# Kernel optimization log

Measured on AMD Instinct MI355X. Metric: run time of the kernel, lower is better.

## Reference

```python
import jax, jax.numpy as jnp
import numpy as np

# Grid derived from defaults: pc_range=(0,-40,-3,70.4,40,1), voxel=(0.2,0.2,4)
GX, GY = 352, 400          # round((70.4-0)/0.2), round((40-(-40))/0.2)
B, P = 4, 65536            # samples, points per sample
NSEG = B * GX * GY + 1     # dense pillar-id space + 1 sentinel for masked points
OUT_CH = 64
BN_EPS = 1e-3


def setup_inputs() -> dict:
    key = jax.random.key(0)
    k1, k2, k3 = jax.random.split(key, 3)
    xyz_min = jnp.array([0.0, -40.0, -3.0], jnp.float32)
    xyz_max = jnp.array([70.4, 40.0, 1.0], jnp.float32)
    xyz = jax.random.uniform(k1, (B, P, 3), jnp.float32, minval=xyz_min, maxval=xyz_max)
    rest = jax.random.normal(k2, (B, P, 4), jnp.float32)  # rcs, v_r, v_r_comp, time
    points = jnp.concatenate([xyz, rest], axis=-1)        # [B, P, 7]
    W = jax.random.normal(k3, (OUT_CH, 13), jnp.float32) * (1.0 / np.sqrt(13.0))
    gamma = jnp.ones((OUT_CH,), jnp.float32)
    beta = jnp.zeros((OUT_CH,), jnp.float32)
    return {"points": points, "W": W, "gamma": gamma, "beta": beta}


def reference(points, W, gamma, beta):
    Bn, Pn, _ = points.shape
    pts = points.reshape(Bn * Pn, 7)                      # [N, 7] (= torch points[:, 1:])
    dtype = pts.dtype
    voxel = jnp.array([0.2, 0.2, 4.0], dtype)
    pc_min = jnp.array([0.0, -40.0, -3.0], dtype)
    batch_idx = jnp.repeat(jnp.arange(Bn, dtype=jnp.int32), Pn)

    coords_f = (pts[:, :3] - pc_min) / voxel              # float voxel coords
    mask = ((coords_f[:, 0] >= 0) & (coords_f[:, 0] < GX)
            & (coords_f[:, 1] >= 0) & (coords_f[:, 1] < GY))
    coords = coords_f.astype(jnp.int32)                   # [N, 3] (cx, cy, cz)
    sentinel = Bn * GX * GY                               # trash segment for masked points
    lin = jnp.where(mask,
                    batch_idx * (GX * GY) + coords[:, 0] * GY + coords[:, 1],
                    sentinel)
    # torch.unique(..., return_inverse=True, dim=0) on (batch, cx, cy) rows ==
    # unique of the bijective linear id (same sorted order).
    unq, unq_inv = jnp.unique(lin, return_inverse=True, size=NSEG, fill_value=sentinel)

    cnt = jax.ops.segment_sum(jnp.ones((lin.shape[0], 1), dtype), unq_inv, num_segments=NSEG)
    mean_xyz = jax.ops.segment_sum(pts[:, :3], unq_inv, num_segments=NSEG) / jnp.maximum(cnt, 1.0)
    f_cluster = pts[:, :3] - mean_xyz[unq_inv]
    f_center = pts[:, :3] - (coords.astype(dtype) * voxel + voxel * 0.5 + pc_min)
    feats = jnp.concatenate([pts, f_cluster, f_center], axis=-1)   # [N, 13]

    # PFN layer (last_layer=True): Linear -> BN1d (training stats) -> ReLU
    x = feats @ W.T                                       # [N, 64]
    mu = x.mean(axis=0)
    var = x.var(axis=0)                                   # biased, as BN training
    x = jax.nn.relu((x - mu) * jax.lax.rsqrt(var + BN_EPS) * gamma + beta)

    fmax = jax.ops.segment_max(x, unq_inv, num_segments=NSEG)     # scatter_max
    x_max = fmax[unq_inv]                                 # gather back (PFN output)
    feat_max = jax.ops.segment_max(x_max, unq_inv, num_segments=NSEG)

    valid = (unq < sentinel)[:, None]                     # real pillars only
    feat_max = jnp.where(valid, feat_max, 0.0)            # padded/empty -> 0

    b = unq // (GX * GY)
    rem = unq % (GX * GY)
    cx = rem // GY
    cy = rem % GY
    coords_out = jnp.stack([b, cy, cx], axis=1).astype(jnp.int32)  # (batch, y, x)
    grid_size = jnp.array([GY, GX], jnp.int32)
    return feat_max, coords_out, grid_size
```

## Files before the change

### kernel.cpp

```cpp
#include <hip/hip_runtime.h>
#include <stdint.h>
#include <utility>

#define NPTS   262144
#define GXGY   140800
#define GYv    400
#define NSEG   563201
#define SENT   563200
#define NB_SCAN 275
#define PIL_BLOCKS 2048

constexpr size_t alignup(size_t x) { return (x + 255) & ~(size_t)255; }
constexpr size_t O_CNT  = 0;
constexpr size_t O_SUMS = alignup(O_CNT + (size_t)NSEG * 4);
constexpr size_t O_MOM  = alignup(O_SUMS + (size_t)NSEG * 12);
constexpr size_t ZERO_BYTES = alignup(O_MOM + 104 * 4);
constexpr size_t O_PPTR = ZERO_BYTES;
constexpr size_t O_LIST = alignup(O_PPTR + (size_t)NSEG * 4);
constexpr size_t O_LINA = alignup(O_LIST + (size_t)NPTS * 4);
constexpr size_t O_FEAT = alignup(O_LINA + (size_t)NPTS * 4);
constexpr size_t O_BSO  = alignup(O_FEAT + (size_t)NPTS * 64);
constexpr size_t O_BSC  = alignup(O_BSO + NB_SCAN * 4);
constexpr size_t O_BOO  = alignup(O_BSC + NB_SCAN * 4);
constexpr size_t O_BOC  = alignup(O_BOO + NB_SCAN * 4);
constexpr size_t O_KP   = alignup(O_BOC + NB_SCAN * 4);
constexpr size_t O_WF   = alignup(O_KP + 256);
constexpr size_t O_SH   = alignup(O_WF + 832 * 4);

__device__ __forceinline__ int point_lin(float x, float y, int b, bool& mask) {
  float cxf = x / 0.2f;
  float cyf = (y + 40.0f) / 0.2f;
  int cx = (int)cxf, cy = (int)cyf;
  mask = (cxf >= 0.0f) && (cxf < 352.0f) && (cyf >= 0.0f) && (cyf < 400.0f);
  return mask ? (b * GXGY + cx * GYv + cy) : SENT;
}

__global__ __launch_bounds__(256) void k_count(const float* __restrict__ pts,
                                               unsigned int* __restrict__ cnt,
                                               float* __restrict__ sums,
                                               unsigned int* __restrict__ lina) {
  int i = blockIdx.x * 256 + threadIdx.x;
  if (i >= NPTS) return;
  const float* p = pts + (size_t)i * 7;
  float x = p[0], y = p[1], z = p[2];
  bool m;
  int lin = point_lin(x, y, i >> 16, m);
  lina[i] = (unsigned)lin;
  atomicAdd(&cnt[lin], 1u);
  atomicAdd(&sums[lin * 3 + 0], x);
  atomicAdd(&sums[lin * 3 + 1], y);
  atomicAdd(&sums[lin * 3 + 2], z);
}

__global__ __launch_bounds__(256) void k_scan1(const unsigned int* __restrict__ cnt,
                                               unsigned int* __restrict__ bso,
                                               unsigned int* __restrict__ bsc) {
  int t = threadIdx.x;
  int base = blockIdx.x * 2048 + t * 8;
  const uint4* c4 = (const uint4*)(cnt + base);
  uint4 a = c4[0], b = c4[1];
  unsigned so = (a.x > 0) + (a.y > 0) + (a.z > 0) + (a.w > 0) +
                (b.x > 0) + (b.y > 0) + (b.z > 0) + (b.w > 0);
  unsigned sc = a.x + a.y + a.z + a.w + b.x + b.y + b.z + b.w;
  for (int m = 1; m < 64; m <<= 1) { so += __shfl_xor(so, m); sc += __shfl_xor(sc, m); }
  __shared__ unsigned wo[4], wc[4];
  if ((t & 63) == 0) { wo[t >> 6] = so; wc[t >> 6] = sc; }
  __syncthreads();
  if (t == 0) {
    bso[blockIdx.x] = wo[0] + wo[1] + wo[2] + wo[3];
    bsc[blockIdx.x] = wc[0] + wc[1] + wc[2] + wc[3];
  }
}

__global__ __launch_bounds__(512) void k_scan2(const unsigned int* __restrict__ bso,
                                               const unsigned int* __restrict__ bsc,
                                               unsigned int* __restrict__ boo,
                                               unsigned int* __restrict__ boc,
                                               unsigned int* __restrict__ kp) {
  int t = threadIdx.x;
  unsigned vo = (t < NB_SCAN) ? bso[t] : 0u;
  unsigned vc = (t < NB_SCAN) ? bsc[t] : 0u;
  __shared__ unsigned so[512], sc[512];
  so[t] = vo; sc[t] = vc;
  __syncthreads();
  for (int off = 1; off < 512; off <<= 1) {
    unsigned ao = (t >= off) ? so[t - off] : 0u;
    unsigned ac = (t >= off) ? sc[t - off] : 0u;
    __syncthreads();
    so[t] += ao; sc[t] += ac;
    __syncthreads();
  }
  if (t < NB_SCAN) { boo[t] = so[t] - vo; boc[t] = sc[t] - vc; }
  if (t == 511) *kp = so[511];
}

__global__ __launch_bounds__(256) void k_scan3(const unsigned int* __restrict__ cnt,
                                               const unsigned int* __restrict__ boo,
                                               const unsigned int* __restrict__ boc,
                                               unsigned int* __restrict__ list,
                                               unsigned int* __restrict__ pptr) {
  int t = threadIdx.x;
  int base = blockIdx.x * 2048 + t * 8;
  const uint4* q = (const uint4*)(cnt + base);
  uint4 a = q[0], b = q[1];
  unsigned c[8] = {a.x, a.y, a.z, a.w, b.x, b.y, b.z, b.w};
  unsigned po[8], pc[8];
  unsigned so = 0, sc = 0;
#pragma unroll
  for (int k = 0; k < 8; k++) {
    po[k] = so; pc[k] = sc;
    so += (c[k] > 0); sc += c[k];
  }
  __shared__ unsigned sdo[256], sdc[256];
  sdo[t] = so; sdc[t] = sc;
  __syncthreads();
  for (int off = 1; off < 256; off <<= 1) {
    unsigned ao = (t >= off) ? sdo[t - off] : 0u;
    unsigned ac = (t >= off) ? sdc[t - off] : 0u;
    __syncthreads();
    sdo[t] += ao; sdc[t] += ac;
    __syncthreads();
  }
  unsigned eo = sdo[t] - so + boo[blockIdx.x];
  unsigned ec = sdc[t] - sc + boc[blockIdx.x];
#pragma unroll
  for (int k = 0; k < 8; k++) {
    if (c[k] > 0) {
      list[eo + po[k]] = base + k;
      pptr[base + k] = ec + pc[k];
    }
  }
}

__global__ __launch_bounds__(256) void k_sortfeat(const float* __restrict__ pts,
                                                  const unsigned int* __restrict__ lina,
                                                  const unsigned int* __restrict__ cnt,
                                                  const float* __restrict__ sums,
                                                  unsigned int* __restrict__ pptr,
                                                  float* __restrict__ feat) {
  int i = blockIdx.x * 256 + threadIdx.x;
  if (i >= NPTS) return;
  unsigned lin = lina[i];
  if (lin == SENT) return;
  const float* p = pts + (size_t)i * 7;
  float x = p[0], y = p[1], z = p[2];
  unsigned pos = atomicAdd(&pptr[lin], 1u);
  float cm = fmaxf((float)cnt[lin], 1.0f);
  float m0 = sums[lin * 3 + 0] / cm;
  float m1 = sums[lin * 3 + 1] / cm;
  float m2 = sums[lin * 3 + 2] / cm;
  int cx = (int)(x / 0.2f);
  int cy = (int)((y + 40.0f) / 0.2f);
  int cz = (int)((z + 3.0f) / 4.0f);
  float4 A = make_float4(x, y, z, p[3]);
  float4 B = make_float4(p[4], p[5], p[6], x - m0);
  float4 C = make_float4(y - m1, z - m2,
                         x - ((float)cx * 0.2f + 0.1f + 0.0f),
                         y - ((float)cy * 0.2f + 0.1f - 40.0f));
  float4 D = make_float4(z - ((float)cz * 4.0f + 2.0f - 3.0f), 0.f, 0.f, 0.f);
  float4* fb = (float4*)(feat + (size_t)pos * 16);
  fb[0] = A; fb[1] = B; fb[2] = C; fb[3] = D;
}

constexpr int tri_j(int t) { int j = 0; while (t >= 13 - j) { t -= 13 - j; j++; } return j; }
constexpr int tri_k(int t) { int j = 0; while (t >= 13 - j) { t -= 13 - j; j++; } return j + t; }

template<int G, size_t U>
__device__ __forceinline__ void accum_one(const float (&f)[13], float (&acc)[52]) {
  constexpr int E = G * 52 + (int)U;
  if constexpr (E < 13) {
    acc[U] += f[E];
  } else {
    constexpr int J = tri_j(E - 13);
    constexpr int K = tri_k(E - 13);
    acc[U] += f[J] * f[K];
  }
}
template<int G, size_t... Us>
__device__ __forceinline__ void accum_all(const float (&f)[13], float (&acc)[52],
                                          std::index_sequence<Us...>) {
  (accum_one<G, Us>(f, acc), ...);
}

template<int G>
__device__ __forceinline__ void moments_body(const float* __restrict__ feat,
                                             float* __restrict__ mom, int chunk) {
  float acc[52];
#pragma unroll
  for (int u = 0; u < 52; u++) acc[u] = 0.f;
#pragma unroll
  for (int r = 0; r < 4; r++) {
    int i = chunk * 1024 + r * 256 + threadIdx.x;
    const float4* fp = (const float4*)(feat + (size_t)i * 16);
    float4 A = fp[0], B = fp[1], C = fp[2], D = fp[3];
    float f[13] = {A.x, A.y, A.z, A.w, B.x, B.y, B.z, B.w, C.x, C.y, C.z, C.w, D.x};
    accum_all<G>(f, acc, std::make_index_sequence<52>{});
  }
  __shared__ float red[4][52];
  int wv = threadIdx.x >> 6, lane = threadIdx.x & 63;
#pragma unroll
  for (int u = 0; u < 52; u++) {
    float v = acc[u];
    v += __shfl_xor(v, 1);  v += __shfl_xor(v, 2);  v += __shfl_xor(v, 4);
    v += __shfl_xor(v, 8);  v += __shfl_xor(v, 16); v += __shfl_xor(v, 32);
    if (lane == 0) red[wv][u] = v;
  }
  __syncthreads();
  if (threadIdx.x < 52) {
    int u = threadIdx.x;
    atomicAdd(&mom[G * 52 + u], red[0][u] + red[1][u] + red[2][u] + red[3][u]);
  }
}

__global__ __launch_bounds__(256, 2) void k_moments(const float* __restrict__ feat,
                                                    float* __restrict__ mom) {
  int chunk = blockIdx.x >> 1;
  if ((blockIdx.x & 1) == 0) moments_body<0>(feat, mom, chunk);
  else                       moments_body<1>(feat, mom, chunk);
}

__global__ void k_bnfinal(const float* __restrict__ W,
                          const float* __restrict__ g,
                          const float* __restrict__ bta,
                          const float* __restrict__ mom,
                          float* __restrict__ wf,
                          float* __restrict__ sh) {
  int c = threadIdx.x;
  float w[13];
#pragma unroll
  for (int j = 0; j < 13; j++) w[j] = W[c * 13 + j];
  const float invN = 1.0f / (float)NPTS;
  float mu = 0.f;
#pragma unroll
  for (int j = 0; j < 13; j++) mu += w[j] * (mom[j] * invN);
  float e2 = 0.f;
  int mi = 13;
#pragma unroll
  for (int j = 0; j < 13; j++) {
#pragma unroll
    for (int k = j; k < 13; k++) {
      float coef = (j == k) ? 1.0f : 2.0f;
      e2 += coef * w[j] * w[k] * mom[mi];
      mi++;
    }
  }
  e2 *= invN;
  float var = e2 - mu * mu;
  float rsig = 1.0f / sqrtf(var + 1e-3f);
  float sc = g[c] * rsig;
#pragma unroll
  for (int j = 0; j < 13; j++) wf[c * 13 + j] = w[j] * sc;
  sh[c] = bta[c] - mu * sc;
}

__global__ __launch_bounds__(256) void k_pillar(const float* __restrict__ wf,
                                                const float* __restrict__ sh,
                                                const unsigned int* __restrict__ cnt,
                                                const unsigned int* __restrict__ pptr,
                                                const unsigned int* __restrict__ list,
                                                const unsigned int* __restrict__ kp_p,
                                                const float* __restrict__ feat,
                                                float* __restrict__ out) {
  int tid = threadIdx.x;
  int lane = tid & 15;
  int ch0 = lane * 4;
  float wr[52];
  float shv[4];
#pragma unroll
  for (int c4 = 0; c4 < 4; c4++) {
    shv[c4] = sh[ch0 + c4];
#pragma unroll
    for (int j = 0; j < 13; j++) wr[c4 * 13 + j] = wf[(ch0 + c4) * 13 + j];
  }
  unsigned kp = *kp_p;

  const int NGRP = PIL_BLOCKS * 16;
  for (int r = blockIdx.x * 16 + (tid >> 4); r < NSEG; r += NGRP) {
    float m0 = -3.4e38f, m1 = -3.4e38f, m2 = -3.4e38f, m3 = -3.4e38f;
    int b = 4, cy = 0, cx = 0;
    if ((unsigned)r < kp) {
      unsigned id = list[r];
      unsigned n = cnt[id];
      unsigned start = pptr[id] - n;
      b = id / GXGY;
      unsigned rem = id - (unsigned)b * GXGY;
      cx = rem / GYv;
      cy = rem - cx * GYv;
      const float4* fb = (const float4*)(feat + (size_t)start * 16);
      for (unsigned p = 0; p < n; p++) {
        float4 A = fb[0], B = fb[1], C = fb[2], D = fb[3];
        fb += 4;
        float d0, d1, d2, d3;
#define DOT(dst, c4)                                                          \
        dst = shv[c4];                                                        \
        dst += wr[c4 * 13 + 0]  * A.x;  dst += wr[c4 * 13 + 1]  * A.y;        \
        dst += wr[c4 * 13 + 2]  * A.z;  dst += wr[c4 * 13 + 3]  * A.w;        \
        dst += wr[c4 * 13 + 4]  * B.x;  dst += wr[c4 * 13 + 5]  * B.y;        \
        dst += wr[c4 * 13 + 6]  * B.z;  dst += wr[c4 * 13 + 7]  * B.w;        \
        dst += wr[c4 * 13 + 8]  * C.x;  dst += wr[c4 * 13 + 9]  * C.y;        \
        dst += wr[c4 * 13 + 10] * C.z;  dst += wr[c4 * 13 + 11] * C.w;        \
        dst += wr[c4 * 13 + 12] * D.x;
        DOT(d0, 0) DOT(d1, 1) DOT(d2, 2) DOT(d3, 3)
#undef DOT
        m0 = fmaxf(m0, d0); m1 = fmaxf(m1, d1);
        m2 = fmaxf(m2, d2); m3 = fmaxf(m3, d3);
      }
    }
    float4 v = make_float4(fmaxf(m0, 0.f), fmaxf(m1, 0.f),
                           fmaxf(m2, 0.f), fmaxf(m3, 0.f));
    *(float4*)(out + (size_t)r * 64 + lane * 4) = v;
    if (lane == 0) {
      float* cc = out + (size_t)NSEG * 64 + (size_t)r * 3;
      cc[0] = (float)b;
      cc[1] = (float)cy;
      cc[2] = (float)cx;
    }
  }
  if (blockIdx.x == 0 && tid == 0) {
    float* g = out + (size_t)NSEG * 67;
    g[0] = 400.0f;
    g[1] = 352.0f;
  }
}

extern "C" void kernel_launch(void* const* d_in, const int* in_sizes, int n_in,
                              void* d_out, int out_size, void* d_ws, size_t ws_size,
                              hipStream_t stream) {
  const float* pts = (const float*)d_in[0];
  const float* W   = (const float*)d_in[1];
  const float* g   = (const float*)d_in[2];
  const float* bta = (const float*)d_in[3];
  float* out = (float*)d_out;
  char* ws = (char*)d_ws;

  unsigned int* cnt  = (unsigned int*)(ws + O_CNT);
  float*        sums = (float*)(ws + O_SUMS);
  float*        mom  = (float*)(ws + O_MOM);
  unsigned int* pptr = (unsigned int*)(ws + O_PPTR);
  unsigned int* list = (unsigned int*)(ws + O_LIST);
  unsigned int* lina = (unsigned int*)(ws + O_LINA);
  float*        feat = (float*)(ws + O_FEAT);
  unsigned int* bso  = (unsigned int*)(ws + O_BSO);
  unsigned int* bsc  = (unsigned int*)(ws + O_BSC);
  unsigned int* boo  = (unsigned int*)(ws + O_BOO);
  unsigned int* boc  = (unsigned int*)(ws + O_BOC);
  unsigned int* kp   = (unsigned int*)(ws + O_KP);
  float*        wf   = (float*)(ws + O_WF);
  float*        sh   = (float*)(ws + O_SH);
  (void)in_sizes; (void)n_in; (void)out_size; (void)ws_size;

  hipMemsetAsync(ws, 0, ZERO_BYTES, stream);

  k_count   <<<NPTS / 256, 256, 0, stream>>>(pts, cnt, sums, lina);
  k_scan1   <<<NB_SCAN, 256, 0, stream>>>(cnt, bso, bsc);
  k_scan2   <<<1, 512, 0, stream>>>(bso, bsc, boo, boc, kp);
  k_scan3   <<<NB_SCAN, 256, 0, stream>>>(cnt, boo, boc, list, pptr);
  k_sortfeat<<<NPTS / 256, 256, 0, stream>>>(pts, lina, cnt, sums, pptr, feat);
  k_moments <<<512, 256, 0, stream>>>(feat, mom);
  k_bnfinal <<<1, 64, 0, stream>>>(W, g, bta, mom, wf, sh);
  k_pillar  <<<PIL_BLOCKS, 256, 0, stream>>>(wf, sh, cnt, pptr, list, kp, feat, out);
}
```

Baseline: 290.1 us.

## Fuse scan offsets into scan3, BN finalize into moments, pack pillar row info

Removes the single-block k_scan2 kernel. Each k_scan3 block now reduces the per-block totals itself to get its own offset and the overall pillar count. The BN finalize step moves into k_moments through a last-block-done atomic counter, and the moments grid is doubled. k_pillar now reads one packed uint4 per row (id, start, count) instead of gathering from the list, count and pointer arrays. The goal is fewer launches, less serialization and fewer dependent loads, at the cost of redundant prefix work in every scan block and a grid-wide fence and atomic in the moments kernel.

```diff
diff --git a/kernel.cpp b/kernel.cpp
--- a/kernel.cpp
+++ b/kernel.cpp
@@ -9,21 +9,21 @@
 #define SENT   563200
 #define NB_SCAN 275
 #define PIL_BLOCKS 2048
+#define MOM_BLOCKS 1024
 
 constexpr size_t alignup(size_t x) { return (x + 255) & ~(size_t)255; }
 constexpr size_t O_CNT  = 0;
 constexpr size_t O_SUMS = alignup(O_CNT + (size_t)NSEG * 4);
 constexpr size_t O_MOM  = alignup(O_SUMS + (size_t)NSEG * 12);
-constexpr size_t ZERO_BYTES = alignup(O_MOM + 104 * 4);
+constexpr size_t O_DONE = alignup(O_MOM + 104 * 4);
+constexpr size_t ZERO_BYTES = alignup(O_DONE + 4);
 constexpr size_t O_PPTR = ZERO_BYTES;
-constexpr size_t O_LIST = alignup(O_PPTR + (size_t)NSEG * 4);
-constexpr size_t O_LINA = alignup(O_LIST + (size_t)NPTS * 4);
-constexpr size_t O_FEAT = alignup(O_LINA + (size_t)NPTS * 4);
+constexpr size_t O_LINA = alignup(O_PPTR + (size_t)NSEG * 4);
+constexpr size_t O_ROWI = alignup(O_LINA + (size_t)NPTS * 4);
+constexpr size_t O_FEAT = alignup(O_ROWI + (size_t)NPTS * 16);
 constexpr size_t O_BSO  = alignup(O_FEAT + (size_t)NPTS * 64);
 constexpr size_t O_BSC  = alignup(O_BSO + NB_SCAN * 4);
-constexpr size_t O_BOO  = alignup(O_BSC + NB_SCAN * 4);
-constexpr size_t O_BOC  = alignup(O_BOO + NB_SCAN * 4);
-constexpr size_t O_KP   = alignup(O_BOC + NB_SCAN * 4);
+constexpr size_t O_KP   = alignup(O_BSC + NB_SCAN * 4);
 constexpr size_t O_WF   = alignup(O_KP + 256);
 constexpr size_t O_SH   = alignup(O_WF + 832 * 4);
 
@@ -72,34 +72,33 @@
   }
 }
 
-__global__ __launch_bounds__(512) void k_scan2(const unsigned int* __restrict__ bso,
+__global__ __launch_bounds__(256) void k_scan3(const unsigned int* __restrict__ cnt,
+                                               const unsigned int* __restrict__ bso,
                                                const unsigned int* __restrict__ bsc,
-                                               unsigned int* __restrict__ boo,
-                                               unsigned int* __restrict__ boc,
+                                               uint4* __restrict__ rowinfo,
+                                               unsigned int* __restrict__ pptr,
                                                unsigned int* __restrict__ kp) {
   int t = threadIdx.x;
-  unsigned vo = (t < NB_SCAN) ? bso[t] : 0u;
-  unsigned vc = (t < NB_SCAN) ? bsc[t] : 0u;
-  __shared__ unsigned so[512], sc[512];
-  so[t] = vo; sc[t] = vc;
-  __syncthreads();
-  for (int off = 1; off < 512; off <<= 1) {
-    unsigned ao = (t >= off) ? so[t - off] : 0u;
-    unsigned ac = (t >= off) ? sc[t - off] : 0u;
-    __syncthreads();
-    so[t] += ao; sc[t] += ac;
-    __syncthreads();
-  }
-  if (t < NB_SCAN) { boo[t] = so[t] - vo; boc[t] = sc[t] - vc; }
-  if (t == 511) *kp = so[511];
-}
-
-__global__ __launch_bounds__(256) void k_scan3(const unsigned int* __restrict__ cnt,
-                                               const unsigned int* __restrict__ boo,
-                                               const unsigned int* __restrict__ boc,
-                                               unsigned int* __restrict__ list,
-                                               unsigned int* __restrict__ pptr) {
-  int t = threadIdx.x;
+  unsigned vo_m = 0, vc_m = 0, vo_a = 0;
+  for (int e = t; e < NB_SCAN; e += 256) {
+    unsigned o = bso[e], c = bsc[e];
+    vo_a += o;
+    if (e < (int)blockIdx.x) { vo_m += o; vc_m += c; }
+  }
+  for (int m = 1; m < 64; m <<= 1) {
+    vo_m += __shfl_xor(vo_m, m);
+    vc_m += __shfl_xor(vc_m, m);
+    vo_a += __shfl_xor(vo_a, m);
+  }
+  __shared__ unsigned s0[4], s1[4], s2[4];
+  int wv = t >> 6;
+  if ((t & 63) == 0) { s0[wv] = vo_m; s1[wv] = vc_m; s2[wv] = vo_a; }
+  __syncthreads();
+  unsigned boo = s0[0] + s0[1] + s0[2] + s0[3];
+  unsigned boc = s1[0] + s1[1] + s1[2] + s1[3];
+  unsigned tot = s2[0] + s2[1] + s2[2] + s2[3];
+  if (blockIdx.x == 0 && t == 0) *kp = tot;
+
   int base = blockIdx.x * 2048 + t * 8;
   const uint4* q = (const uint4*)(cnt + base);
   uint4 a = q[0], b = q[1];
@@ -112,6 +111,7 @@
     so += (c[k] > 0); sc += c[k];
   }
   __shared__ unsigned sdo[256], sdc[256];
+  __syncthreads();
   sdo[t] = so; sdc[t] = sc;
   __syncthreads();
   for (int off = 1; off < 256; off <<= 1) {
@@ -121,13 +121,15 @@
     sdo[t] += ao; sdc[t] += ac;
     __syncthreads();
   }
-  unsigned eo = sdo[t] - so + boo[blockIdx.x];
-  unsigned ec = sdc[t] - sc + boc[blockIdx.x];
+  unsigned eo = sdo[t] - so + boo;
+  unsigned ec = sdc[t] - sc + boc;
 #pragma unroll
   for (int k = 0; k < 8; k++) {
     if (c[k] > 0) {
-      list[eo + po[k]] = base + k;
-      pptr[base + k] = ec + pc[k];
+      unsigned r = eo + po[k];
+      unsigned start = ec + pc[k];
+      rowinfo[r] = make_uint4((unsigned)(base + k), start, c[k], 0u);
+      pptr[base + k] = start;
     }
   }
 }
@@ -213,51 +215,60 @@
 }
 
 __global__ __launch_bounds__(256, 2) void k_moments(const float* __restrict__ feat,
-                                                    float* __restrict__ mom) {
+                                                    float* __restrict__ mom,
+                                                    unsigned int* __restrict__ done,
+                                                    const float* __restrict__ W,
+                                                    const float* __restrict__ g,
+                                                    const float* __restrict__ bta,
+                                                    float* __restrict__ wf,
+                                                    float* __restrict__ sh) {
   int chunk = blockIdx.x >> 1;
   if ((blockIdx.x & 1) == 0) moments_body<0>(feat, mom, chunk);
   else                       moments_body<1>(feat, mom, chunk);
-}
-
-__global__ void k_bnfinal(const float* __restrict__ W,
-                          const float* __restrict__ g,
-                          const float* __restrict__ bta,
-                          const float* __restrict__ mom,
-                          float* __restrict__ wf,
-                          float* __restrict__ sh) {
-  int c = threadIdx.x;
-  float w[13];
-#pragma unroll
-  for (int j = 0; j < 13; j++) w[j] = W[c * 13 + j];
-  const float invN = 1.0f / (float)NPTS;
-  float mu = 0.f;
-#pragma unroll
-  for (int j = 0; j < 13; j++) mu += w[j] * (mom[j] * invN);
-  float e2 = 0.f;
-  int mi = 13;
-#pragma unroll
-  for (int j = 0; j < 13; j++) {
-#pragma unroll
-    for (int k = j; k < 13; k++) {
-      float coef = (j == k) ? 1.0f : 2.0f;
-      e2 += coef * w[j] * w[k] * mom[mi];
-      mi++;
+
+  __threadfence();
+  __shared__ unsigned lastFlag;
+  if (threadIdx.x == 0)
+    lastFlag = (atomicAdd(done, 1u) == (unsigned)(gridDim.x - 1)) ? 1u : 0u;
+  __syncthreads();
+  if (!lastFlag) return;
+
+  __shared__ float lm[104];
+  int t = threadIdx.x;
+  if (t < 104) lm[t] = atomicAdd(&mom[t], 0.0f);
+  __syncthreads();
+  if (t < 64) {
+    float w[13];
+#pragma unroll
+    for (int j = 0; j < 13; j++) w[j] = W[t * 13 + j];
+    const float invN = 1.0f / (float)NPTS;
+    float mu = 0.f;
+#pragma unroll
+    for (int j = 0; j < 13; j++) mu += w[j] * (lm[j] * invN);
+    float e2 = 0.f;
+    int mi = 13;
+#pragma unroll
+    for (int j = 0; j < 13; j++) {
+#pragma unroll
+      for (int k = j; k < 13; k++) {
+        float coef = (j == k) ? 1.0f : 2.0f;
+        e2 += coef * w[j] * w[k] * lm[mi];
+        mi++;
+      }
     }
-  }
-  e2 *= invN;
-  float var = e2 - mu * mu;
-  float rsig = 1.0f / sqrtf(var + 1e-3f);
-  float sc = g[c] * rsig;
-#pragma unroll
-  for (int j = 0; j < 13; j++) wf[c * 13 + j] = w[j] * sc;
-  sh[c] = bta[c] - mu * sc;
+    e2 *= invN;
+    float var = e2 - mu * mu;
+    float rsig = 1.0f / sqrtf(var + 1e-3f);
+    float sc = g[t] * rsig;
+#pragma unroll
+    for (int j = 0; j < 13; j++) wf[t * 13 + j] = w[j] * sc;
+    sh[t] = bta[t] - mu * sc;
+  }
 }
 
 __global__ __launch_bounds__(256) void k_pillar(const float* __restrict__ wf,
                                                 const float* __restrict__ sh,
-                                                const unsigned int* __restrict__ cnt,
-                                                const unsigned int* __restrict__ pptr,
-                                                const unsigned int* __restrict__ list,
+                                                const uint4* __restrict__ rowinfo,
                                                 const unsigned int* __restrict__ kp_p,
                                                 const float* __restrict__ feat,
                                                 float* __restrict__ out) {
@@ -279,9 +290,8 @@
     float m0 = -3.4e38f, m1 = -3.4e38f, m2 = -3.4e38f, m3 = -3.4e38f;
     int b = 4, cy = 0, cx = 0;
     if ((unsigned)r < kp) {
-      unsigned id = list[r];
-      unsigned n = cnt[id];
-      unsigned start = pptr[id] - n;
+      uint4 ri = rowinfo[r];
+      unsigned id = ri.x, start = ri.y, n = ri.z;
       b = id / GXGY;
       unsigned rem = id - (unsigned)b * GXGY;
       cx = rem / GYv;
@@ -336,14 +346,13 @@
   unsigned int* cnt  = (unsigned int*)(ws + O_CNT);
   float*        sums = (float*)(ws + O_SUMS);
   float*        mom  = (float*)(ws + O_MOM);
+  unsigned int* done = (unsigned int*)(ws + O_DONE);
   unsigned int* pptr = (unsigned int*)(ws + O_PPTR);
-  unsigned int* list = (unsigned int*)(ws + O_LIST);
   unsigned int* lina = (unsigned int*)(ws + O_LINA);
+  uint4*        rowi = (uint4*)(ws + O_ROWI);
   float*        feat = (float*)(ws + O_FEAT);
   unsigned int* bso  = (unsigned int*)(ws + O_BSO);
   unsigned int* bsc  = (unsigned int*)(ws + O_BSC);
-  unsigned int* boo  = (unsigned int*)(ws + O_BOO);
-  unsigned int* boc  = (unsigned int*)(ws + O_BOC);
   unsigned int* kp   = (unsigned int*)(ws + O_KP);
   float*        wf   = (float*)(ws + O_WF);
   float*        sh   = (float*)(ws + O_SH);
@@ -353,10 +362,8 @@
 
   k_count   <<<NPTS / 256, 256, 0, stream>>>(pts, cnt, sums, lina);
   k_scan1   <<<NB_SCAN, 256, 0, stream>>>(cnt, bso, bsc);
-  k_scan2   <<<1, 512, 0, stream>>>(bso, bsc, boo, boc, kp);
-  k_scan3   <<<NB_SCAN, 256, 0, stream>>>(cnt, boo, boc, list, pptr);
+  k_scan3   <<<NB_SCAN, 256, 0, stream>>>(cnt, bso, bsc, rowi, pptr, kp);
   k_sortfeat<<<NPTS / 256, 256, 0, stream>>>(pts, lina, cnt, sums, pptr, feat);
-  k_moments <<<512, 256, 0, stream>>>(feat, mom);
-  k_bnfinal <<<1, 64, 0, stream>>>(W, g, bta, mom, wf, sh);
-  k_pillar  <<<PIL_BLOCKS, 256, 0, stream>>>(wf, sh, cnt, pptr, list, kp, feat, out);
-}
+  k_moments <<<MOM_BLOCKS, 256, 0, stream>>>(feat, mom, done, W, g, bta, wf, sh);
+  k_pillar  <<<PIL_BLOCKS, 256, 0, stream>>>(wf, sh, rowi, kp, feat, out);
+}
```

After: 335.3 us. 1.16x slower.
